# Kernel tuning notes

Measured on AMD Instinct MI355X. Metric: run time of the kernel, lower is better.

Reference implementation:

```python
import jax, jax.numpy as jnp
import numpy as np


def setup_inputs() -> dict:
    key0 = jax.random.key(0)
    k1, k2, k3, k4 = jax.random.split(key0, 4)
    bs, h, S, dk = 4, 16, 2048, 64
    query = jax.random.normal(k1, (bs * h, S, dk), dtype=jnp.float32)
    key = jax.random.normal(k2, (bs * h, S, dk), dtype=jnp.float32)
    value = jax.random.normal(k3, (bs * h, S, dk), dtype=jnp.float32)
    attn_mask = jax.random.randint(k4, (bs, S), 0, 2, dtype=jnp.int64)
    return {"query": query, "key": key, "value": value, "attn_mask": attn_mask}


def reference(query, key, value, attn_mask):
    bs_h, K, dk = key.shape
    Q = query.shape[1]
    bs = attn_mask.shape[0]
    h = bs_h // bs
    # [bs_h, Q, K] scores, scaled by sqrt(d_k)
    scores = jnp.einsum('bqd,bkd->bqk', query, key) / jnp.sqrt(jnp.asarray(dk, query.dtype))
    # mask==0 positions get an additive -1e-10 (faithful to original, incl. its tiny magnitude)
    m = (attn_mask == 0).astype(scores.dtype)          # [bs, K]
    m = jnp.tile(m, (h, 1))[:, None, :]                # [bs_h, 1, K] (torch .repeat(h,1) tiles)
    scores = scores + m * (-1e-10)
    attn = jax.nn.softmax(scores, axis=-1)
    # dropout p=0.0 (identity in this deterministic reference)
    return jnp.einsum('bqk,bkd->bqd', attn, value)
```

## Files before the change

### kernel.cpp

```cpp
#include <hip/hip_runtime.h>
#include <hip/hip_bf16.h>
#include <stdint.h>

typedef __bf16 bf16x8 __attribute__((ext_vector_type(8)));
typedef float  f32x4  __attribute__((ext_vector_type(4)));
typedef float  f32x16 __attribute__((ext_vector_type(16)));
typedef int    i32x2  __attribute__((ext_vector_type(2)));
typedef unsigned short u16x8 __attribute__((ext_vector_type(8)));
typedef unsigned short u16x4 __attribute__((ext_vector_type(4)));

#define S_LEN 2048
#define DK    64
#define KVBLK 64
#define NT    (S_LEN / KVBLK)
#define QW    32
#define QBLK  128
#define TILE_E (KVBLK * DK)

static __device__ __forceinline__ unsigned short f2bf(float f) {
    union { float f; unsigned u; } v; v.f = f;
    unsigned r = v.u + 0x7fffu + ((v.u >> 16) & 1u);
    return (unsigned short)(r >> 16);
}

static __device__ __forceinline__ float fexp2(float x) {
#if __has_builtin(__builtin_amdgcn_exp2f)
    return __builtin_amdgcn_exp2f(x);
#else
    return exp2f(x);
#endif
}

static __device__ __forceinline__ unsigned cvtpk(float lo, float hi) {
    unsigned r;
    asm("v_cvt_pk_bf16_f32 %0, %1, %2" : "=v"(r) : "v"(lo), "v"(hi));
    return r;
}

static __device__ __forceinline__ i32x2 plswap(int a, int b) {
#if __has_builtin(__builtin_amdgcn_permlane32_swap)
    return __builtin_amdgcn_permlane32_swap(a, b, false, false);
#else
    const bool up = (threadIdx.x & 32) != 0;
    int as = __shfl_xor(a, 32, 64);
    int bs = __shfl_xor(b, 32, 64);
    i32x2 r;
    r[0] = up ? bs : a;
    r[1] = up ? b  : as;
    return r;
#endif
}
static __device__ __forceinline__ float xhalf_sum(float x) {
    union { float f; int i; } u; u.f = x;
    i32x2 t = plswap(u.i, u.i);
    union { int i; float f; } a, b; a.i = t[0]; b.i = t[1];
    return a.f + b.f;
}

__global__ __launch_bounds__(256)
void conv_all(const float* __restrict__ Q, const float* __restrict__ K,
              const float* __restrict__ V,
              unsigned short* __restrict__ Qb, unsigned short* __restrict__ Kb,
              unsigned short* __restrict__ Vb, int tiles) {
    __shared__ unsigned short tile[KVBLK][DK + 2];
    const int b = blockIdx.x;
    const int tid = threadIdx.x;
    if (b < tiles) {
        const float* src = K + (size_t)b * TILE_E;
        unsigned short* dst = Kb + (size_t)b * TILE_E;
        #pragma unroll
        for (int g = 0; g < 2; ++g) {
            const int p = tid * 8 + g * 2048;
            const int k = p >> 6;
            const int d = (p ^ ((k & 7) << 3)) & 63;
            const float* s = src + k * DK + d;
            u16x8 o;
            #pragma unroll
            for (int j = 0; j < 8; ++j) o[j] = f2bf(s[j]);
            *(u16x8*)&dst[p] = o;
        }
    } else if (b < 2 * tiles) {
        const int bb = b - tiles;
        const float* src = V + (size_t)bb * TILE_E;
        const int k = tid >> 2, c = (tid & 3) * 16;
        #pragma unroll
        for (int j = 0; j < 16; ++j) tile[k][c + j] = f2bf(src[k * DK + c + j]);
        __syncthreads();
        unsigned short* dst = Vb + (size_t)bb * TILE_E;
        #pragma unroll
        for (int g = 0; g < 2; ++g) {
            const int p = tid * 8 + g * 2048;
            const int d = p >> 6;
            const int k0 = (p ^ ((d & 7) << 3)) & 63;
            u16x8 o;
            #pragma unroll
            for (int j = 0; j < 8; ++j) o[j] = tile[k0 + j][d];
            *(u16x8*)&dst[p] = o;
        }
    } else {
        const size_t i = ((size_t)(b - 2 * tiles) * 256 + tid) * 8;
        const float4 v0 = *(const float4*)(Q + i);
        const float4 v1 = *(const float4*)(Q + i + 4);
        const float s = 0.125f * 1.44269504089f;
        u16x8 o;
        o[0] = f2bf(v0.x * s); o[1] = f2bf(v0.y * s);
        o[2] = f2bf(v0.z * s); o[3] = f2bf(v0.w * s);
        o[4] = f2bf(v1.x * s); o[5] = f2bf(v1.y * s);
        o[6] = f2bf(v1.z * s); o[7] = f2bf(v1.w * s);
        *(u16x8*)&Qb[i] = o;
    }
}


__global__ __launch_bounds__(256)
void sdpa_fwd2(const unsigned short* __restrict__ Qb,
               const unsigned short* __restrict__ Kb,
               const unsigned short* __restrict__ Vb,
               float* __restrict__ O) {
    __shared__ __align__(16) char smem[32768];

    const int tid  = threadIdx.x;
    const int lane = tid & 63;
    const int wave = tid >> 6;
    const int ln   = lane & 31;
    const int hi   = lane >> 5;

    const int head = blockIdx.y;
    const int q0   = blockIdx.x * QBLK + wave * QW;

    const unsigned short* KbH = Kb + (size_t)head * NT * TILE_E;
    const unsigned short* VbH = Vb + (size_t)head * NT * TILE_E;

    u16x8 qfrag[4];
    {
        const unsigned short* qsrc = Qb + ((size_t)head * S_LEN + q0 + ln) * DK + hi * 8;
        #pragma unroll
        for (int ds = 0; ds < 4; ++ds) qfrag[ds] = *(const u16x8*)&qsrc[ds * 16];
    }

    auto STAGE = [&](int t, int b) {
        const unsigned short* Kt = KbH + (size_t)t * TILE_E;
        const unsigned short* Vt = VbH + (size_t)t * TILE_E;
        unsigned short* sKb = (unsigned short*)(smem + b * 16384);
        unsigned short* sVb = (unsigned short*)(smem + b * 16384 + 8192);
        #pragma unroll
        for (int i = 0; i < 2; ++i) {
            __builtin_amdgcn_global_load_lds(
                (const __attribute__((address_space(1))) void*)(Kt + i * 2048 + tid * 8),
                (__attribute__((address_space(3))) void*)(&sKb[i * 2048 + wave * 512]),
                16, 0, 0);
            __builtin_amdgcn_global_load_lds(
                (const __attribute__((address_space(1))) void*)(Vt + i * 2048 + tid * 8),
                (__attribute__((address_space(3))) void*)(&sVb[i * 2048 + wave * 512]),
                16, 0, 0);
        }
    };

    f32x16 oacc[2];
    #pragma unroll
    for (int dblk = 0; dblk < 2; ++dblk)
        #pragma unroll
        for (int r = 0; r < 16; ++r) oacc[dblk][r] = 0.0f;
    float lsum = 0.0f;

    STAGE(0, 0);

    #pragma unroll 2
    for (int t = 0; t < NT; ++t) {
        const int cur = t & 1;
        if (t + 1 < NT) {
            STAGE(t + 1, cur ^ 1);
            asm volatile("s_waitcnt vmcnt(4)" ::: "memory");
        } else {
            asm volatile("s_waitcnt vmcnt(0)" ::: "memory");
        }
        __builtin_amdgcn_s_barrier();
        __builtin_amdgcn_sched_barrier(0);

        const unsigned short* sK  = (const unsigned short*)(smem + cur * 16384);
        const unsigned short* sVT = (const unsigned short*)(smem + cur * 16384 + 8192);

        f32x16 sacc[2];
        #pragma unroll
        for (int sub = 0; sub < 2; ++sub)
            #pragma unroll
            for (int r = 0; r < 16; ++r) sacc[sub][r] = 0.0f;
        __builtin_amdgcn_s_setprio(1);
        #pragma unroll
        for (int sub = 0; sub < 2; ++sub) {
            const int k   = sub * 32 + ln;
            const int swz = (k & 7) << 3;
            #pragma unroll
            for (int ds = 0; ds < 4; ++ds) {
                u16x8 kf = *(const u16x8*)&sK[(k * DK + ds * 16 + hi * 8) ^ swz];
                sacc[sub] = __builtin_amdgcn_mfma_f32_32x32x16_bf16(
                    __builtin_bit_cast(bf16x8, kf), __builtin_bit_cast(bf16x8, qfrag[ds]),
                    sacc[sub], 0, 0, 0);
            }
        }
        __builtin_amdgcn_s_setprio(0);

        float s0 = 0.f, s1 = 0.f, s2 = 0.f, s3 = 0.f;
        #pragma unroll
        for (int sub = 0; sub < 2; ++sub)
            #pragma unroll
            for (int i = 0; i < 16; i += 4) {
                float e0 = fexp2(sacc[sub][i]);
                float e1 = fexp2(sacc[sub][i + 1]);
                float e2 = fexp2(sacc[sub][i + 2]);
                float e3 = fexp2(sacc[sub][i + 3]);
                sacc[sub][i] = e0; sacc[sub][i + 1] = e1;
                sacc[sub][i + 2] = e2; sacc[sub][i + 3] = e3;
                s0 += e0; s1 += e1; s2 += e2; s3 += e3;
            }
        lsum += (s0 + s1) + (s2 + s3);

        u16x8 pa[2][2];
        #pragma unroll
        for (int sub = 0; sub < 2; ++sub) {
            unsigned w[8];
            #pragma unroll
            for (int i = 0; i < 8; ++i)
                w[i] = cvtpk(sacc[sub][2 * i], sacc[sub][2 * i + 1]);
            i32x2 a0 = plswap((int)w[0], (int)w[2]);
            i32x2 a1 = plswap((int)w[1], (int)w[3]);
            i32x2 a2 = plswap((int)w[4], (int)w[6]);
            i32x2 a3 = plswap((int)w[5], (int)w[7]);
            unsigned pk0[4] = { (unsigned)a0[0], (unsigned)a1[0], (unsigned)a0[1], (unsigned)a1[1] };
            unsigned pk1[4] = { (unsigned)a2[0], (unsigned)a3[0], (unsigned)a2[1], (unsigned)a3[1] };
            pa[sub][0] = *(u16x8*)pk0;
            pa[sub][1] = *(u16x8*)pk1;
        }

        __builtin_amdgcn_s_setprio(1);
        #pragma unroll
        for (int sub = 0; sub < 2; ++sub)
            #pragma unroll
            for (int dblk = 0; dblk < 2; ++dblk) {
                const int d   = dblk * 32 + ln;
                const int swz = (d & 7) << 3;
                #pragma unroll
                for (int ks = 0; ks < 2; ++ks) {
                    u16x8 vf = *(const u16x8*)&sVT[(d * KVBLK + sub * 32 + ks * 16 + hi * 8) ^ swz];
                    oacc[dblk] = __builtin_amdgcn_mfma_f32_32x32x16_bf16(
                        __builtin_bit_cast(bf16x8, vf), __builtin_bit_cast(bf16x8, pa[sub][ks]),
                        oacc[dblk], 0, 0, 0);
                }
            }
        __builtin_amdgcn_s_setprio(0);

        __builtin_amdgcn_s_barrier();
    }

    const float inv = 1.0f / xhalf_sum(lsum);

    float* tp = (float*)smem + wave * (64 * 32);
    __syncthreads();
    #pragma unroll
    for (int dblk = 0; dblk < 2; ++dblk)
        #pragma unroll
        for (int r = 0; r < 16; ++r) {
            const int d = dblk * 32 + (r & 3) + 8 * (r >> 2) + 4 * hi;
            tp[d * 32 + ln] = oacc[dblk][r] * inv;
        }
    __syncthreads();
    {
        const int qloc = lane >> 1;
        const int dh   = (lane & 1) * 32;
        float* Orow = O + ((size_t)head * S_LEN + q0 + qloc) * DK + dh;
        #pragma unroll
        for (int c = 0; c < 8; ++c) {
            float4 v;
            v.x = tp[(dh + c * 4 + 0) * 32 + qloc];
            v.y = tp[(dh + c * 4 + 1) * 32 + qloc];
            v.z = tp[(dh + c * 4 + 2) * 32 + qloc];
            v.w = tp[(dh + c * 4 + 3) * 32 + qloc];
            *(float4*)(Orow + c * 4) = v;
        }
    }
}


__global__ __launch_bounds__(256)
void sdpa_fwd_fb(const float* __restrict__ Q, const float* __restrict__ K,
                 const float* __restrict__ V, float* __restrict__ O) {
    __shared__ unsigned short sK[KVBLK * DK];
    __shared__ unsigned short sVT[DK * KVBLK];
    __shared__ unsigned short sP[4][16 * KVBLK];
    const int tid = threadIdx.x, lane = tid & 63, wave = tid >> 6;
    const int lo = lane & 15, hi = lane >> 4;
    const int head = blockIdx.y;
    const int q0 = blockIdx.x * 64 + wave * 16;
    const float* Qh = Q + (size_t)head * S_LEN * DK;
    const float* Kh = K + (size_t)head * S_LEN * DK;
    const float* Vh = V + (size_t)head * S_LEN * DK;
    bf16x8 qfrag[2];
    {
        const int qrow = q0 + lo;
        for (int ks = 0; ks < 2; ++ks) {
            const float* p = Qh + (size_t)qrow * DK + ks * 32 + hi * 8;
            u16x8 u;
            #pragma unroll
            for (int j = 0; j < 8; ++j) u[j] = f2bf(p[j] * 0.125f);
            qfrag[ks] = __builtin_bit_cast(bf16x8, u);
        }
    }
    f32x4 oacc[4];
    #pragma unroll
    for (int dc = 0; dc < 4; ++dc) for (int i = 0; i < 4; ++i) oacc[dc][i] = 0.0f;
    float mrow[4] = {-1e30f, -1e30f, -1e30f, -1e30f};
    float lrow[4] = {0.f, 0.f, 0.f, 0.f};
    for (int kv = 0; kv < S_LEN; kv += KVBLK) {
        {
            const int k = tid >> 2, c = tid & 3;
            const float* src = Kh + (size_t)(kv + k) * DK + c * 16;
            u16x8 a, b;
            #pragma unroll
            for (int j = 0; j < 8; ++j) a[j] = f2bf(src[j]);
            #pragma unroll
            for (int j = 0; j < 8; ++j) b[j] = f2bf(src[8 + j]);
            const int sw = (k & 7) << 3, base = k * DK + c * 16;
            *(u16x8*)&sK[(base) ^ sw] = a;
            *(u16x8*)&sK[(base + 8) ^ sw] = b;
        }
        {
            const int d = tid & 63, sw = (d & 7) << 3;
            #pragma unroll
            for (int half = 0; half < 2; ++half) {
                const int k0 = (tid >> 6) * 8 + half * 32;
                u16x8 v;
                #pragma unroll
                for (int j = 0; j < 8; ++j) v[j] = f2bf(Vh[(size_t)(kv + k0 + j) * DK + d]);
                *(u16x8*)&sVT[(d * KVBLK + k0) ^ sw] = v;
            }
        }
        __syncthreads();
        f32x4 sacc[4];
        #pragma unroll
        for (int kc = 0; kc < 4; ++kc) for (int i = 0; i < 4; ++i) sacc[kc][i] = 0.0f;
        #pragma unroll
        for (int kc = 0; kc < 4; ++kc) {
            const int krow = kc * 16 + lo, sw = (krow & 7) << 3;
            #pragma unroll
            for (int ks = 0; ks < 2; ++ks) {
                u16x8 u = *(const u16x8*)&sK[(krow * DK + ks * 32 + hi * 8) ^ sw];
                sacc[kc] = __builtin_amdgcn_mfma_f32_16x16x32_bf16(
                    qfrag[ks], __builtin_bit_cast(bf16x8, u), sacc[kc], 0, 0, 0);
            }
        }
        float pv[4][4], mnew[4], sc[4];
        #pragma unroll
        for (int r = 0; r < 4; ++r) {
            float t = fmaxf(fmaxf(sacc[0][r], sacc[1][r]), fmaxf(sacc[2][r], sacc[3][r]));
            #pragma unroll
            for (int mm = 1; mm <= 8; mm <<= 1) t = fmaxf(t, __shfl_xor(t, mm, 64));
            mnew[r] = fmaxf(mrow[r], t);
            sc[r] = __expf(mrow[r] - mnew[r]);
        }
        #pragma unroll
        for (int r = 0; r < 4; ++r) {
            float s = 0.f;
            #pragma unroll
            for (int kc = 0; kc < 4; ++kc) { float e = __expf(sacc[kc][r] - mnew[r]); pv[kc][r] = e; s += e; }
            #pragma unroll
            for (int mm = 1; mm <= 8; mm <<= 1) s += __shfl_xor(s, mm, 64);
            lrow[r] = lrow[r] * sc[r] + s;
            mrow[r] = mnew[r];
        }
        #pragma unroll
        for (int dc = 0; dc < 4; ++dc)
            #pragma unroll
            for (int r = 0; r < 4; ++r) oacc[dc][r] *= sc[r];
        unsigned short* sPw = sP[wave];
        #pragma unroll
        for (int r = 0; r < 4; ++r) {
            const int row = hi * 4 + r, sw = (row & 7) << 3;
            #pragma unroll
            for (int kc = 0; kc < 4; ++kc)
                sPw[(row * KVBLK + kc * 16 + lo) ^ sw] = f2bf(pv[kc][r]);
        }
        bf16x8 pfrag[2];
        {
            const int sw = (lo & 7) << 3;
            #pragma unroll
            for (int ks = 0; ks < 2; ++ks) {
                u16x8 u = *(const u16x8*)&sPw[(lo * KVBLK + ks * 32 + hi * 8) ^ sw];
                pfrag[ks] = __builtin_bit_cast(bf16x8, u);
            }
        }
        #pragma unroll
        for (int dc = 0; dc < 4; ++dc) {
            const int d = dc * 16 + lo, sw = (d & 7) << 3;
            #pragma unroll
            for (int ks = 0; ks < 2; ++ks) {
                u16x8 u = *(const u16x8*)&sVT[(d * KVBLK + ks * 32 + hi * 8) ^ sw];
                oacc[dc] = __builtin_amdgcn_mfma_f32_16x16x32_bf16(
                    pfrag[ks], __builtin_bit_cast(bf16x8, u), oacc[dc], 0, 0, 0);
            }
        }
        __syncthreads();
    }
    float* Oh = O + (size_t)head * S_LEN * DK;
    #pragma unroll
    for (int r = 0; r < 4; ++r) {
        const float inv = 1.0f / lrow[r];
        const int row = q0 + hi * 4 + r;
        #pragma unroll
        for (int dc = 0; dc < 4; ++dc)
            Oh[(size_t)row * DK + dc * 16 + lo] = oacc[dc][r] * inv;
    }
}

extern "C" void kernel_launch(void* const* d_in, const int* in_sizes, int n_in,
                              void* d_out, int out_size, void* d_ws, size_t ws_size,
                              hipStream_t stream) {
    const float* Q = (const float*)d_in[0];
    const float* K = (const float*)d_in[1];
    const float* V = (const float*)d_in[2];
    float* O = (float*)d_out;
    const int heads = in_sizes[0] / (S_LEN * DK);
    const size_t n  = (size_t)heads * S_LEN * DK;
    const size_t need = 3 * n * sizeof(unsigned short);

    if (ws_size >= need) {
        unsigned short* Qb = (unsigned short*)d_ws;
        unsigned short* Kb = Qb + n;
        unsigned short* Vb = Kb + n;
        const int tiles = (int)(n / TILE_E);
        const int qblocks = (int)(n / 8 / 256);
        conv_all<<<2 * tiles + qblocks, 256, 0, stream>>>(Q, K, V, Qb, Kb, Vb, tiles);
        dim3 grid(S_LEN / QBLK, heads);
        sdpa_fwd2<<<grid, 256, 0, stream>>>(Qb, Kb, Vb, O);
    } else {
        dim3 grid(S_LEN / 64, heads);
        sdpa_fwd_fb<<<grid, 256, 0, stream>>>(Q, K, V, O);
    }
}
```

Before: 117.1 us.

## Process two 32-row query blocks per wave to reuse K/V fragments

Each wave now handles 64 query rows as two 32-row blocks, so the block covers 256 queries. Every K and V fragment read from LDS feeds two MFMAs, which halves LDS reads and global K/V staging per query. This halves the grid size and roughly doubles accumulator and score register use, which may lower occupancy or cause spills. The epilogue writes the two blocks one after the other through shared memory, with extra syncs.

```diff
diff --git a/kernel.cpp b/kernel.cpp
--- a/kernel.cpp
+++ b/kernel.cpp
@@ -13,8 +13,7 @@
 #define DK    64
 #define KVBLK 64
 #define NT    (S_LEN / KVBLK)
-#define QW    32
-#define QBLK  128
+#define QBLK  256
 #define TILE_E (KVBLK * DK)
 
 static __device__ __forceinline__ unsigned short f2bf(float f) {
@@ -126,16 +125,18 @@
     const int hi   = lane >> 5;
 
     const int head = blockIdx.y;
-    const int q0   = blockIdx.x * QBLK + wave * QW;
+    const int q0w  = blockIdx.x * QBLK + wave * 64;
 
     const unsigned short* KbH = Kb + (size_t)head * NT * TILE_E;
     const unsigned short* VbH = Vb + (size_t)head * NT * TILE_E;
 
-    u16x8 qfrag[4];
-    {
-        const unsigned short* qsrc = Qb + ((size_t)head * S_LEN + q0 + ln) * DK + hi * 8;
-        #pragma unroll
-        for (int ds = 0; ds < 4; ++ds) qfrag[ds] = *(const u16x8*)&qsrc[ds * 16];
+    u16x8 qfrag[2][4];
+    #pragma unroll
+    for (int qb = 0; qb < 2; ++qb) {
+        const unsigned short* qsrc =
+            Qb + ((size_t)head * S_LEN + q0w + qb * 32 + ln) * DK + hi * 8;
+        #pragma unroll
+        for (int ds = 0; ds < 4; ++ds) qfrag[qb][ds] = *(const u16x8*)&qsrc[ds * 16];
     }
 
     auto STAGE = [&](int t, int b) {
@@ -156,12 +157,14 @@
         }
     };
 
-    f32x16 oacc[2];
+    f32x16 oacc[2][2];
     #pragma unroll
-    for (int dblk = 0; dblk < 2; ++dblk)
-        #pragma unroll
-        for (int r = 0; r < 16; ++r) oacc[dblk][r] = 0.0f;
-    float lsum = 0.0f;
+    for (int qb = 0; qb < 2; ++qb)
+        #pragma unroll
+        for (int dblk = 0; dblk < 2; ++dblk)
+            #pragma unroll
+            for (int r = 0; r < 16; ++r) oacc[qb][dblk][r] = 0.0f;
+    float lsum0 = 0.0f, lsum1 = 0.0f;
 
     STAGE(0, 0);
 
@@ -180,11 +183,13 @@
         const unsigned short* sK  = (const unsigned short*)(smem + cur * 16384);
         const unsigned short* sVT = (const unsigned short*)(smem + cur * 16384 + 8192);
 
-        f32x16 sacc[2];
-        #pragma unroll
-        for (int sub = 0; sub < 2; ++sub)
-            #pragma unroll
-            for (int r = 0; r < 16; ++r) sacc[sub][r] = 0.0f;
+        f32x16 sacc[2][2];
+        #pragma unroll
+        for (int qb = 0; qb < 2; ++qb)
+            #pragma unroll
+            for (int sub = 0; sub < 2; ++sub)
+                #pragma unroll
+                for (int r = 0; r < 16; ++r) sacc[qb][sub][r] = 0.0f;
         __builtin_amdgcn_s_setprio(1);
         #pragma unroll
         for (int sub = 0; sub < 2; ++sub) {
@@ -193,43 +198,50 @@
             #pragma unroll
             for (int ds = 0; ds < 4; ++ds) {
                 u16x8 kf = *(const u16x8*)&sK[(k * DK + ds * 16 + hi * 8) ^ swz];
-                sacc[sub] = __builtin_amdgcn_mfma_f32_32x32x16_bf16(
-                    __builtin_bit_cast(bf16x8, kf), __builtin_bit_cast(bf16x8, qfrag[ds]),
-                    sacc[sub], 0, 0, 0);
+                sacc[0][sub] = __builtin_amdgcn_mfma_f32_32x32x16_bf16(
+                    __builtin_bit_cast(bf16x8, kf), __builtin_bit_cast(bf16x8, qfrag[0][ds]),
+                    sacc[0][sub], 0, 0, 0);
+                sacc[1][sub] = __builtin_amdgcn_mfma_f32_32x32x16_bf16(
+                    __builtin_bit_cast(bf16x8, kf), __builtin_bit_cast(bf16x8, qfrag[1][ds]),
+                    sacc[1][sub], 0, 0, 0);
             }
         }
         __builtin_amdgcn_s_setprio(0);
 
-        float s0 = 0.f, s1 = 0.f, s2 = 0.f, s3 = 0.f;
-        #pragma unroll
-        for (int sub = 0; sub < 2; ++sub)
-            #pragma unroll
-            for (int i = 0; i < 16; i += 4) {
-                float e0 = fexp2(sacc[sub][i]);
-                float e1 = fexp2(sacc[sub][i + 1]);
-                float e2 = fexp2(sacc[sub][i + 2]);
-                float e3 = fexp2(sacc[sub][i + 3]);
-                sacc[sub][i] = e0; sacc[sub][i + 1] = e1;
-                sacc[sub][i + 2] = e2; sacc[sub][i + 3] = e3;
-                s0 += e0; s1 += e1; s2 += e2; s3 += e3;
-            }
-        lsum += (s0 + s1) + (s2 + s3);
-
-        u16x8 pa[2][2];
-        #pragma unroll
-        for (int sub = 0; sub < 2; ++sub) {
-            unsigned w[8];
-            #pragma unroll
-            for (int i = 0; i < 8; ++i)
-                w[i] = cvtpk(sacc[sub][2 * i], sacc[sub][2 * i + 1]);
-            i32x2 a0 = plswap((int)w[0], (int)w[2]);
-            i32x2 a1 = plswap((int)w[1], (int)w[3]);
-            i32x2 a2 = plswap((int)w[4], (int)w[6]);
-            i32x2 a3 = plswap((int)w[5], (int)w[7]);
-            unsigned pk0[4] = { (unsigned)a0[0], (unsigned)a1[0], (unsigned)a0[1], (unsigned)a1[1] };
-            unsigned pk1[4] = { (unsigned)a2[0], (unsigned)a3[0], (unsigned)a2[1], (unsigned)a3[1] };
-            pa[sub][0] = *(u16x8*)pk0;
-            pa[sub][1] = *(u16x8*)pk1;
+        u16x8 pa[2][2][2];
+        #pragma unroll
+        for (int qb = 0; qb < 2; ++qb) {
+            float s0 = 0.f, s1 = 0.f, s2 = 0.f, s3 = 0.f;
+            #pragma unroll
+            for (int sub = 0; sub < 2; ++sub)
+                #pragma unroll
+                for (int i = 0; i < 16; i += 4) {
+                    float e0 = fexp2(sacc[qb][sub][i]);
+                    float e1 = fexp2(sacc[qb][sub][i + 1]);
+                    float e2 = fexp2(sacc[qb][sub][i + 2]);
+                    float e3 = fexp2(sacc[qb][sub][i + 3]);
+                    sacc[qb][sub][i] = e0; sacc[qb][sub][i + 1] = e1;
+                    sacc[qb][sub][i + 2] = e2; sacc[qb][sub][i + 3] = e3;
+                    s0 += e0; s1 += e1; s2 += e2; s3 += e3;
+                }
+            const float part = (s0 + s1) + (s2 + s3);
+            if (qb == 0) lsum0 += part; else lsum1 += part;
+
+            #pragma unroll
+            for (int sub = 0; sub < 2; ++sub) {
+                unsigned w[8];
+                #pragma unroll
+                for (int i = 0; i < 8; ++i)
+                    w[i] = cvtpk(sacc[qb][sub][2 * i], sacc[qb][sub][2 * i + 1]);
+                i32x2 a0 = plswap((int)w[0], (int)w[2]);
+                i32x2 a1 = plswap((int)w[1], (int)w[3]);
+                i32x2 a2 = plswap((int)w[4], (int)w[6]);
+                i32x2 a3 = plswap((int)w[5], (int)w[7]);
+                unsigned pk0[4] = { (unsigned)a0[0], (unsigned)a1[0], (unsigned)a0[1], (unsigned)a1[1] };
+                unsigned pk1[4] = { (unsigned)a2[0], (unsigned)a3[0], (unsigned)a2[1], (unsigned)a3[1] };
+                pa[qb][sub][0] = *(u16x8*)pk0;
+                pa[qb][sub][1] = *(u16x8*)pk1;
+            }
         }
 
         __builtin_amdgcn_s_setprio(1);
@@ -242,9 +254,12 @@
                 #pragma unroll
                 for (int ks = 0; ks < 2; ++ks) {
                     u16x8 vf = *(const u16x8*)&sVT[(d * KVBLK + sub * 32 + ks * 16 + hi * 8) ^ swz];
-                    oacc[dblk] = __builtin_amdgcn_mfma_f32_32x32x16_bf16(
-                        __builtin_bit_cast(bf16x8, vf), __builtin_bit_cast(bf16x8, pa[sub][ks]),
-                        oacc[dblk], 0, 0, 0);
+                    oacc[0][dblk] = __builtin_amdgcn_mfma_f32_32x32x16_bf16(
+                        __builtin_bit_cast(bf16x8, vf), __builtin_bit_cast(bf16x8, pa[0][sub][ks]),
+                        oacc[0][dblk], 0, 0, 0);
+                    oacc[1][dblk] = __builtin_amdgcn_mfma_f32_32x32x16_bf16(
+                        __builtin_bit_cast(bf16x8, vf), __builtin_bit_cast(bf16x8, pa[1][sub][ks]),
+                        oacc[1][dblk], 0, 0, 0);
                 }
             }
         __builtin_amdgcn_s_setprio(0);
@@ -252,22 +267,23 @@
         __builtin_amdgcn_s_barrier();
     }
 
-    const float inv = 1.0f / xhalf_sum(lsum);
-
-    float* tp = (float*)smem + wave * (64 * 32);
-    __syncthreads();
+    const float inv[2] = { 1.0f / xhalf_sum(lsum0), 1.0f / xhalf_sum(lsum1) };
+
+    float* tp = (float*)(smem + wave * 8192);
     #pragma unroll
-    for (int dblk = 0; dblk < 2; ++dblk)
-        #pragma unroll
-        for (int r = 0; r < 16; ++r) {
-            const int d = dblk * 32 + (r & 3) + 8 * (r >> 2) + 4 * hi;
-            tp[d * 32 + ln] = oacc[dblk][r] * inv;
-        }
-    __syncthreads();
-    {
+    for (int qb = 0; qb < 2; ++qb) {
+        __syncthreads();
+        #pragma unroll
+        for (int dblk = 0; dblk < 2; ++dblk)
+            #pragma unroll
+            for (int r = 0; r < 16; ++r) {
+                const int d = dblk * 32 + (r & 3) + 8 * (r >> 2) + 4 * hi;
+                tp[d * 32 + ln] = oacc[qb][dblk][r] * inv[qb];
+            }
+        __syncthreads();
         const int qloc = lane >> 1;
         const int dh   = (lane & 1) * 32;
-        float* Orow = O + ((size_t)head * S_LEN + q0 + qloc) * DK + dh;
+        float* Orow = O + ((size_t)head * S_LEN + q0w + qb * 32 + qloc) * DK + dh;
         #pragma unroll
         for (int c = 0; c < 8; ++c) {
             float4 v;
```

After: 129.4 us. 1.1x slower.
